# Performance work log

Hardware: AMD Instinct MI355X
Metric: run time of the kernel (lower is better)

## Reference

```python
import jax, jax.numpy as jnp
import numpy as np

B, N_OBJ, N_REL = 32, 100, 512
D_OBJ, D_CTX, D_HID = 1024, 1024, 1024


def setup_inputs() -> dict:
    key = jax.random.key(0)
    k1, k2, k3, k4, k5 = jax.random.split(key, 5)
    object_branch_output = jax.random.normal(k1, (B * N_OBJ, D_OBJ), dtype=jnp.float32)
    context_branch_output = jax.random.normal(k2, (B, D_CTX), dtype=jnp.float32)
    num_obj = jnp.full((B,), N_OBJ, dtype=jnp.int32)
    num_rels = jnp.full((B,), N_REL, dtype=jnp.int32)
    obj_pairs = jax.random.randint(k3, (B, N_REL, 2), 0, N_OBJ, dtype=jnp.int32)
    W1 = jax.random.normal(k4, (D_OBJ + D_CTX, D_HID), dtype=jnp.float32) * (1.0 / np.sqrt(D_OBJ + D_CTX))
    b1 = jnp.zeros((D_HID,), dtype=jnp.float32)
    W2 = jax.random.normal(k5, (D_HID, D_HID), dtype=jnp.float32) * (1.0 / np.sqrt(D_HID))
    b2 = jnp.zeros((D_HID,), dtype=jnp.float32)
    return {
        "object_branch_output": object_branch_output,
        "context_branch_output": context_branch_output,
        "num_obj": num_obj,
        "num_rels": num_rels,
        "obj_pairs": obj_pairs,
        "W1": W1, "b1": b1, "W2": W2, "b2": b2,
    }


def reference(object_branch_output, context_branch_output, num_obj, num_rels,
              obj_pairs, W1, b1, W2, b2):
    # --- prepare_f_oo_vis_input, fully vectorized ---
    # per-batch object index offsets: sum(num_obj[:b])  (exclusive cumsum)
    obj_offsets = jnp.cumsum(num_obj) - num_obj                       # [B]
    global_pairs = obj_pairs + obj_offsets[:, None, None]             # [B, R, 2]
    # gather both endpoints of every pair and mean-aggregate
    pair_feats = object_branch_output[global_pairs]                   # [B, R, 2, D_obj]
    obj_vec = pair_feats.mean(axis=2)                                 # [B, R, D_obj]
    # broadcast per-batch context vector to every relation, then concat
    ctx = jnp.broadcast_to(context_branch_output[:, None, :],
                           obj_vec.shape[:2] + (context_branch_output.shape[-1],))
    input_f_oo_vis = jnp.concatenate([obj_vec, ctx], axis=-1)         # [B, R, D_obj+D_ctx]
    x = input_f_oo_vis.reshape(-1, input_f_oo_vis.shape[-1])          # [tot_rels, D_obj+D_ctx]
    # --- f_oo_vis MLP: (Linear -> ReLU) per layer pair ---
    h = jax.nn.relu(x @ W1 + b1)
    f_oo_vis_output = jax.nn.relu(h @ W2 + b2)
    return object_branch_output, f_oo_vis_output
```

## Files before the change

kernel.cpp:

```cpp
#include <hip/hip_runtime.h>
#include <hip/hip_bf16.h>

#define BB   32
#define NREL 512
#define DD   1024
#define MTOT (BB * NREL)
#define OBJ_ROWS (BB * 100)

typedef __attribute__((ext_vector_type(8))) short bf16x8;
typedef __attribute__((ext_vector_type(4))) float f32x4;

__device__ __forceinline__ unsigned short f2bf(float f) {
    union { float f; unsigned u; } v; v.f = f;
    unsigned r = v.u + 0x7fff + ((v.u >> 16) & 1);
    return (unsigned short)(r >> 16);
}

__device__ __forceinline__ void gld16(const void* g, void* l) {
    __builtin_amdgcn_global_load_lds(
        (const __attribute__((address_space(1))) unsigned int*)g,
        (__attribute__((address_space(3))) unsigned int*)l,
        16, 0, 0);
}

__device__ __forceinline__ void barfence() {
    asm volatile("" ::: "memory");
    __builtin_amdgcn_s_barrier();
    asm volatile("" ::: "memory");
}

__global__ void __launch_bounds__(256) prep_kernel(
    const float* __restrict__ obj, const float* __restrict__ ctx,
    const int* __restrict__ num_obj, const int* __restrict__ pairs,
    const float* __restrict__ W1, const float* __restrict__ b1,
    const float* __restrict__ W2,
    unsigned short* __restrict__ W1t, unsigned short* __restrict__ W2t,
    float* __restrict__ cp, unsigned short* __restrict__ objvec,
    float* __restrict__ out_obj) {
    __shared__ float smem[32 * 33];
    int bid = blockIdx.x;
    int tid = threadIdx.x;

    if (bid < 256) {
        int b = bid >> 3, chunk = bid & 7;
        int nl = tid & 127, kh = tid >> 7;
        int n = chunk * 128 + nl;
        const float* c = ctx + (size_t)b * DD + kh * 512;
        const float* w = W1 + (size_t)(DD + kh * 512) * DD + n;
        float a0 = 0.f, a1 = 0.f, a2 = 0.f, a3 = 0.f;
#pragma unroll 4
        for (int k = 0; k < 512; k += 4) {
            a0 = fmaf(c[k + 0], w[(size_t)(k + 0) * DD], a0);
            a1 = fmaf(c[k + 1], w[(size_t)(k + 1) * DD], a1);
            a2 = fmaf(c[k + 2], w[(size_t)(k + 2) * DD], a2);
            a3 = fmaf(c[k + 3], w[(size_t)(k + 3) * DD], a3);
        }
        smem[kh * 128 + nl] = (a0 + a1) + (a2 + a3);
        __syncthreads();
        if (kh == 0) cp[(size_t)b * DD + n] = smem[nl] + smem[128 + nl] + b1[n];
    } else if (bid < 2304) {
        const float* W = (bid < 1280) ? W1 : W2;
        unsigned short* Wt = (bid < 1280) ? W1t : W2t;
        int t = (bid - 256) & 1023;
        int k0 = (t >> 5) * 32, n0 = (t & 31) * 32;
        int tr = tid >> 5, tc = tid & 31;
#pragma unroll
        for (int i = 0; i < 4; i++)
            smem[(tr + i * 8) * 33 + tc] = W[(size_t)(k0 + tr + i * 8) * DD + n0 + tc];
        __syncthreads();
#pragma unroll
        for (int i = 0; i < 4; i++)
            Wt[(size_t)(n0 + tr + i * 8) * DD + k0 + tc] = f2bf(smem[tc * 33 + tr + i * 8]);
    } else if (bid < 6400) {
        int rbase = (bid - 2304) * 4;
        int b = rbase >> 9;
        int off = 0;
        for (int i = 0; i < b; i++) off += num_obj[i];
#pragma unroll
        for (int rr = 0; rr < 4; rr++) {
            int row = rbase + rr;
            int i0 = pairs[2 * row] + off;
            int i1 = pairs[2 * row + 1] + off;
            float4 x = ((const float4*)obj)[(size_t)i0 * (DD / 4) + tid];
            float4 y = ((const float4*)obj)[(size_t)i1 * (DD / 4) + tid];
            ushort4 o;
            o.x = f2bf(0.5f * (x.x + y.x));
            o.y = f2bf(0.5f * (x.y + y.y));
            o.z = f2bf(0.5f * (x.z + y.z));
            o.w = f2bf(0.5f * (x.w + y.w));
            ((ushort4*)(objvec + (size_t)row * DD))[tid] = o;
        }
    } else {
        const float4* src = (const float4*)obj;
        float4* dst = (float4*)out_obj;
        for (int i = (bid - 6400) * 256 + tid; i < OBJ_ROWS * DD / 4; i += 2048 * 256)
            dst[i] = src[i];
    }
}

template <int MODE>
__global__ void __launch_bounds__(512, 2) gemm256_kernel(
    const unsigned short* __restrict__ A,
    const unsigned short* __restrict__ Bt,
    const float* __restrict__ bias,
    void* __restrict__ Cout) {
    constexpr int K = 1024;
    constexpr int NT = K / 64;
    extern __shared__ unsigned short lds[];
    int tid = threadIdx.x;
    int lane = tid & 63, wave = tid >> 6;
    int wr = wave >> 2, wc = wave & 3;
    int lr = lane & 15, g = lane >> 4;

    int wg = blockIdx.x;
    int swz = (wg & 7) * 32 + (wg >> 3);
    int mBase = (swz >> 2) * 256;
    int nBase = (swz & 3) * 256;

    const unsigned short* Ab = A + (size_t)mBase * K;
    const unsigned short* Bb = Bt + (size_t)nBase * K;

    int srow[4], soff[4], sdst[4];
#pragma unroll
    for (int i = 0; i < 4; i++) {
        int s = i * 512 + tid;
        int row = s >> 3, cperm = s & 7;
        srow[i] = row;
        soff[i] = (cperm ^ (row & 7)) * 8;
        sdst[i] = s * 8;
    }

    f32x4 acc[8][4];
#pragma unroll
    for (int i = 0; i < 8; i++)
#pragma unroll
        for (int j = 0; j < 4; j++) acc[i][j] = (f32x4){0.f, 0.f, 0.f, 0.f};

    auto STAGE = [&](int bi, int kt) {
        unsigned short* Ad = lds + bi * 16384;
        unsigned short* Bd = lds + 32768 + bi * 16384;
        int ko = kt * 64;
#pragma unroll
        for (int i = 0; i < 4; i++) {
            gld16(Ab + (size_t)srow[i] * K + ko + soff[i], Ad + sdst[i]);
            gld16(Bb + (size_t)srow[i] * K + ko + soff[i], Bd + sdst[i]);
        }
    };

    auto COMPUTE = [&](int bi) {
        const unsigned short* As = lds + bi * 16384;
        const unsigned short* Bs = lds + 32768 + bi * 16384;
        bf16x8 bfr[4][2];
#pragma unroll
        for (int n = 0; n < 4; n++)
#pragma unroll
            for (int kk = 0; kk < 2; kk++) {
                int row = wc * 64 + n * 16 + lr;
                int c = kk * 4 + g;
                bfr[n][kk] = *(const bf16x8*)&Bs[row * 64 + ((c ^ (row & 7)) * 8)];
            }
#pragma unroll
        for (int half = 0; half < 2; half++) {
            bf16x8 af[4][2];
#pragma unroll
            for (int m = 0; m < 4; m++)
#pragma unroll
                for (int kk = 0; kk < 2; kk++) {
                    int row = wr * 128 + (half * 4 + m) * 16 + lr;
                    int c = kk * 4 + g;
                    af[m][kk] = *(const bf16x8*)&As[row * 64 + ((c ^ (row & 7)) * 8)];
                }
            __builtin_amdgcn_s_setprio(1);
#pragma unroll
            for (int m = 0; m < 4; m++)
#pragma unroll
                for (int n = 0; n < 4; n++)
#pragma unroll
                    for (int kk = 0; kk < 2; kk++)
                        acc[half * 4 + m][n] = __builtin_amdgcn_mfma_f32_16x16x32_bf16(
                            af[m][kk], bfr[n][kk], acc[half * 4 + m][n], 0, 0, 0);
            __builtin_amdgcn_s_setprio(0);
        }
    };

    STAGE(0, 0);
    int cur = 0;
    for (int kt = 0; kt < NT - 1; ++kt) {
        STAGE(cur ^ 1, kt + 1);
        asm volatile("s_waitcnt vmcnt(8)" ::: "memory");
        barfence();
        COMPUTE(cur);
        barfence();
        cur ^= 1;
    }
    asm volatile("s_waitcnt vmcnt(0)" ::: "memory");
    barfence();
    COMPUTE(cur);

    int rg = g * 4;
    int bbase = (mBase >> 9) << 10;
#pragma unroll
    for (int m = 0; m < 8; m++) {
#pragma unroll
        for (int n = 0; n < 4; n++) {
            int col = nBase + wc * 64 + n * 16 + lr;
            float bv = (MODE == 1) ? bias[bbase + col] : bias[col];
#pragma unroll
            for (int r = 0; r < 4; r++) {
                int row = mBase + wr * 128 + m * 16 + rg + r;
                float v = acc[m][n][r] + bv;
                v = v > 0.f ? v : 0.f;
                if (MODE == 1)
                    ((unsigned short*)Cout)[(size_t)row * 1024 + col] = f2bf(v);
                else
                    ((float*)Cout)[(size_t)row * 1024 + col] = v;
            }
        }
    }
}

extern "C" void kernel_launch(void* const* d_in, const int* in_sizes, int n_in,
                              void* d_out, int out_size, void* d_ws, size_t ws_size,
                              hipStream_t stream) {
    (void)in_sizes; (void)n_in; (void)out_size; (void)ws_size;
    const float* obj     = (const float*)d_in[0];
    const float* ctx     = (const float*)d_in[1];
    const int*   num_obj = (const int*)d_in[2];
    const int*   pairs   = (const int*)d_in[4];
    const float* W1      = (const float*)d_in[5];
    const float* b1      = (const float*)d_in[6];
    const float* W2      = (const float*)d_in[7];
    const float* b2      = (const float*)d_in[8];

    char* ws = (char*)d_ws;
    unsigned short* objvec = (unsigned short*)(ws);
    unsigned short* h      = (unsigned short*)(ws + 33554432);
    unsigned short* W1t    = (unsigned short*)(ws + 67108864);
    unsigned short* W2t    = (unsigned short*)(ws + 69206016);
    float*          cp     = (float*)(ws + 71303168);

    float* out_obj = (float*)d_out;
    float* out_f   = out_obj + (size_t)OBJ_ROWS * DD;

    hipFuncSetAttribute(reinterpret_cast<const void*>(gemm256_kernel<1>),
                        hipFuncAttributeMaxDynamicSharedMemorySize, 131072);
    hipFuncSetAttribute(reinterpret_cast<const void*>(gemm256_kernel<2>),
                        hipFuncAttributeMaxDynamicSharedMemorySize, 131072);

    prep_kernel<<<dim3(8448), 256, 0, stream>>>(
        obj, ctx, num_obj, pairs, W1, b1, W2, W1t, W2t, cp, objvec, out_obj);
    gemm256_kernel<1><<<dim3(256), 512, 131072, stream>>>(objvec, W1t, cp, (void*)h);
    gemm256_kernel<2><<<dim3(256), 512, 131072, stream>>>(h, W2t, b2, (void*)out_f);
}
```

Before: 105.1 us.

## Split per-tile MFMA compute into four quadrants with barrier-interleaved LDS reads

Restructures the inner GEMM loop so each K-tile runs as four quadrant phases (2x2 over M halves and N halves). Each phase loads only the A/B fragments it needs from LDS and is bracketed by workgroup barriers, in the style of ping-pong scheduling, so waves alternate between LDS reads and MFMA bursts. The last tile is folded into the main loop. The extra barriers per tile add synchronization overhead and can serialize waves if the interleaving does not pay off.

```diff
diff --git a/kernel.cpp b/kernel.cpp
--- a/kernel.cpp
+++ b/kernel.cpp
@@ -147,55 +147,58 @@
         }
     };
 
-    auto COMPUTE = [&](int bi) {
-        const unsigned short* As = lds + bi * 16384;
-        const unsigned short* Bs = lds + 32768 + bi * 16384;
-        bf16x8 bfr[4][2];
-#pragma unroll
-        for (int n = 0; n < 4; n++)
-#pragma unroll
-            for (int kk = 0; kk < 2; kk++) {
-                int row = wc * 64 + n * 16 + lr;
-                int c = kk * 4 + g;
-                bfr[n][kk] = *(const bf16x8*)&Bs[row * 64 + ((c ^ (row & 7)) * 8)];
-            }
-#pragma unroll
-        for (int half = 0; half < 2; half++) {
-            bf16x8 af[4][2];
-#pragma unroll
-            for (int m = 0; m < 4; m++)
-#pragma unroll
-                for (int kk = 0; kk < 2; kk++) {
-                    int row = wr * 128 + (half * 4 + m) * 16 + lr;
-                    int c = kk * 4 + g;
-                    af[m][kk] = *(const bf16x8*)&As[row * 64 + ((c ^ (row & 7)) * 8)];
-                }
-            __builtin_amdgcn_s_setprio(1);
-#pragma unroll
-            for (int m = 0; m < 4; m++)
-#pragma unroll
-                for (int n = 0; n < 4; n++)
-#pragma unroll
-                    for (int kk = 0; kk < 2; kk++)
-                        acc[half * 4 + m][n] = __builtin_amdgcn_mfma_f32_16x16x32_bf16(
-                            af[m][kk], bfr[n][kk], acc[half * 4 + m][n], 0, 0, 0);
-            __builtin_amdgcn_s_setprio(0);
-        }
-    };
-
     STAGE(0, 0);
     int cur = 0;
-    for (int kt = 0; kt < NT - 1; ++kt) {
-        STAGE(cur ^ 1, kt + 1);
-        asm volatile("s_waitcnt vmcnt(8)" ::: "memory");
+    for (int kt = 0; kt < NT; ++kt) {
+        const unsigned short* As = lds + cur * 16384;
+        const unsigned short* Bs = lds + 32768 + cur * 16384;
+        if (kt + 1 < NT) {
+            STAGE(cur ^ 1, kt + 1);
+            asm volatile("s_waitcnt vmcnt(8)" ::: "memory");
+        } else {
+            asm volatile("s_waitcnt vmcnt(0)" ::: "memory");
+        }
         barfence();
-        COMPUTE(cur);
-        barfence();
+
+        bf16x8 af[4][2], bfa[4][2];
+#pragma unroll
+        for (int q = 0; q < 4; ++q) {
+            const int qm = q >> 1, qn = q & 1;
+            if (q == 0 || q == 2) {
+#pragma unroll
+                for (int m = 0; m < 4; m++)
+#pragma unroll
+                    for (int kk = 0; kk < 2; kk++) {
+                        int row = wr * 128 + (qm * 4 + m) * 16 + lr;
+                        int c = kk * 4 + g;
+                        af[m][kk] = *(const bf16x8*)&As[row * 64 + ((c ^ (row & 7)) * 8)];
+                    }
+            }
+            if (q < 2) {
+#pragma unroll
+                for (int n = 0; n < 2; n++)
+#pragma unroll
+                    for (int kk = 0; kk < 2; kk++) {
+                        int row = wc * 64 + (qn * 2 + n) * 16 + lr;
+                        int c = kk * 4 + g;
+                        bfa[qn * 2 + n][kk] = *(const bf16x8*)&Bs[row * 64 + ((c ^ (row & 7)) * 8)];
+                    }
+            }
+            barfence();
+            __builtin_amdgcn_s_setprio(1);
+#pragma unroll
+            for (int m = 0; m < 4; m++)
+#pragma unroll
+                for (int n = 0; n < 2; n++)
+#pragma unroll
+                    for (int kk = 0; kk < 2; kk++)
+                        acc[qm * 4 + m][qn * 2 + n] = __builtin_amdgcn_mfma_f32_16x16x32_bf16(
+                            af[m][kk], bfa[qn * 2 + n][kk], acc[qm * 4 + m][qn * 2 + n], 0, 0, 0);
+            __builtin_amdgcn_s_setprio(0);
+            barfence();
+        }
         cur ^= 1;
     }
-    asm volatile("s_waitcnt vmcnt(0)" ::: "memory");
-    barfence();
-    COMPUTE(cur);
 
     int rg = g * 4;
     int bbase = (mBase >> 9) << 10;
```

Result: slower. 109.2 us (+3.8%).
